# Kernel tuning notes

Measured on AMD Instinct MI355X. Metric: run time of the kernel, lower is better.

## Reference

```python
import jax, jax.numpy as jnp
import numpy as np


def setup_inputs() -> dict:
    key = jax.random.key(0)
    k1, k2, k3 = jax.random.split(key, 3)
    N, D, H, E = 8192, 1024, 1024, 16
    scale = 1.0 / np.sqrt(D)
    return {
        "x": jax.random.normal(k1, (N, D), dtype=jnp.float32),
        "router_w": jax.random.normal(k2, (D, E), dtype=jnp.float32) * scale,
        "router_b": jnp.zeros((E,), dtype=jnp.float32),
        "expert_w": jax.random.normal(k3, (E, D, H), dtype=jnp.float32) * scale,
        "expert_b": jnp.zeros((E, H), dtype=jnp.float32),
        "k": 2,
    }


def reference(x, router_w, router_b, expert_w, expert_b, k):
    # Router: softmax over experts, then top-k.
    logits = x @ router_w + router_b                      # [N, E]
    routing_weights = jax.nn.softmax(logits, axis=-1)     # [N, E]
    top_k_weights, top_k_indices = jax.lax.top_k(routing_weights, k)  # [N, k]

    # Dense all-expert compute (faithful to original): [N, E, H]
    expert_outputs = jnp.einsum('nd,edh->neh', x, expert_w) + expert_b[None, :, :]

    # Gather top-k expert outputs: [N, k, H]
    gathered = jnp.take_along_axis(expert_outputs, top_k_indices[:, :, None], axis=1)

    # Weighted sum over k (weights NOT renormalized, as in the original).
    out = jnp.sum(top_k_weights[:, :, None] * gathered, axis=1)  # [N, H]
    return out
```

## Files before the change

kernel.cpp:

```cpp
#include <hip/hip_runtime.h>
#include <hip/hip_bf16.h>


#define N_TOK 8192
#define D_DIM 1024
#define H_DIM 1024
#define E_NUM 16
#define CAP   1024
#define KPAD  40

typedef __attribute__((ext_vector_type(4))) float f32x4;
typedef __attribute__((ext_vector_type(8))) short bf16x8;

__device__ __forceinline__ unsigned short f2bf(float f) {
    unsigned int u = __float_as_uint(f);
    unsigned int r = u + 0x7fffu + ((u >> 16) & 1u);
    return (unsigned short)(r >> 16);
}
__device__ __forceinline__ unsigned int pk2bf(float lo, float hi) {
    return (unsigned int)f2bf(lo) | ((unsigned int)f2bf(hi) << 16);
}

__global__ __launch_bounds__(256) void router_lds(
    const float* __restrict__ x,
    const float* __restrict__ rw,
    const float* __restrict__ rb,
    int4* __restrict__ res,
    unsigned short* __restrict__ xb)
{
    __shared__ __align__(16) float xls[8][4][260];
    __shared__ double lg[4][2][E_NUM];

    const int tid = threadIdx.x;
    const int t0b = blockIdx.x * 8;

    {
        const int r   = tid >> 5;
        const int c32 = (tid & 31) * 32;
        const int s   = c32 >> 8;
        const int p0  = c32 & 255;
        const float* src = x + (size_t)(t0b + r) * D_DIM + c32;
        float4 v[8];
#pragma unroll
        for (int j = 0; j < 8; ++j) v[j] = *(const float4*)(src + j * 4);
#pragma unroll
        for (int j = 0; j < 8; ++j)
            *(float4*)&xls[r][s][p0 + j * 4] = v[j];
        unsigned int q[16];
#pragma unroll
        for (int j = 0; j < 8; ++j) {
            q[2 * j]     = pk2bf(v[j].x, v[j].y);
            q[2 * j + 1] = pk2bf(v[j].z, v[j].w);
        }
        unsigned short* dst = xb + (size_t)(t0b + r) * D_DIM + c32;
        *(uint4*)(dst)      = *(uint4*)&q[0];
        *(uint4*)(dst + 8)  = *(uint4*)&q[4];
        *(uint4*)(dst + 16) = *(uint4*)&q[8];
        *(uint4*)(dst + 24) = *(uint4*)&q[12];
    }
    __syncthreads();

    const int wave = tid >> 6;
    const int lane = tid & 63;
    const int ds   = lane >> 4;
    const int e    = lane & 15;
    const int lr0  = wave * 2;
    const float* rwp = rw + ds * 4096 + e;

    double acc0 = 0.0, acc1 = 0.0;
#pragma unroll 2
    for (int g = 0; g < 8; ++g) {
        float s0 = 0.0f, s1 = 0.0f;
#pragma unroll
        for (int u = 0; u < 8; ++u) {
            const int jb = g * 8 + u;
            const float4 a = *(const float4*)&xls[lr0][ds][jb * 4];
            const float4 b = *(const float4*)&xls[lr0 + 1][ds][jb * 4];
            const float w0 = rwp[jb * 64];
            const float w1 = rwp[jb * 64 + 16];
            const float w2 = rwp[jb * 64 + 32];
            const float w3 = rwp[jb * 64 + 48];
            s0 = fmaf(a.w, w3, fmaf(a.z, w2, fmaf(a.y, w1, fmaf(a.x, w0, s0))));
            s1 = fmaf(b.w, w3, fmaf(b.z, w2, fmaf(b.y, w1, fmaf(b.x, w0, s1))));
        }
        acc0 += (double)s0;
        acc1 += (double)s1;
    }

    double v0 = acc0, v1 = acc1;
    v0 += __shfl_xor(v0, 16); v0 += __shfl_xor(v0, 32);
    v1 += __shfl_xor(v1, 16); v1 += __shfl_xor(v1, 32);

    if (ds == 0) {
        const double bias = (double)rb[e];
        lg[wave][0][e] = v0 + bias;
        lg[wave][1][e] = v1 + bias;
    }
    __syncthreads();

    if (lane < 2) {
        const double* L = lg[wave][lane];
        double m = L[0];
#pragma unroll
        for (int k = 1; k < E_NUM; ++k) m = fmax(m, L[k]);

        int e1 = 0;
#pragma unroll
        for (int k = 1; k < E_NUM; ++k) if (L[k] > L[e1]) e1 = k;
        int e2 = (e1 == 0) ? 1 : 0;
        for (int k = 0; k < E_NUM; ++k)
            if (k != e1 && L[k] > L[e2]) e2 = k;

        float s = 0.0f;
#pragma unroll
        for (int k = 0; k < E_NUM; ++k) s = fmaf(expf((float)(L[k] - m)), 1.0f, s);
        const float w1 = expf((float)(L[e1] - m)) / s;
        const float w2 = expf((float)(L[e2] - m)) / s;

        const int n = t0b + wave * 2 + lane;
        res[n] = make_int4(e1, e2, __float_as_int(w1), __float_as_int(w2));
    }
}

template <bool WRITE_XB>
__global__ __launch_bounds__(256, 4) void router_kernel(
    const float* __restrict__ x,
    const float* __restrict__ rw,
    const float* __restrict__ rb,
    int4* __restrict__ res,
    unsigned short* __restrict__ xb)
{
    const int wave = threadIdx.x >> 6;
    const int lane = threadIdx.x & 63;
    const int ds   = lane >> 4;
    const int e    = lane & 15;
    const int t0   = blockIdx.x * 8 + wave * 2;

    const float* x0  = x + (size_t)t0 * D_DIM + ds * 256;
    const float* x1  = x0 + D_DIM;
    const float* rwp = rw + ds * 4096 + e;

    double acc0 = 0.0, acc1 = 0.0;
#pragma unroll 2
    for (int g = 0; g < 8; ++g) {
        float s0 = 0.0f, s1 = 0.0f;
#pragma unroll
        for (int u = 0; u < 8; ++u) {
            const int jb = g * 8 + u;
            const float4 a = *(const float4*)(x0 + jb * 4);
            const float4 b = *(const float4*)(x1 + jb * 4);
            const float w0 = rwp[jb * 64];
            const float w1 = rwp[jb * 64 + 16];
            const float w2 = rwp[jb * 64 + 32];
            const float w3 = rwp[jb * 64 + 48];
            s0 = fmaf(a.w, w3, fmaf(a.z, w2, fmaf(a.y, w1, fmaf(a.x, w0, s0))));
            s1 = fmaf(b.w, w3, fmaf(b.z, w2, fmaf(b.y, w1, fmaf(b.x, w0, s1))));
        }
        acc0 += (double)s0;
        acc1 += (double)s1;
    }

    if (WRITE_XB) {
#pragma unroll
        for (int t = 0; t < 2; ++t) {
            const float* src = x + (size_t)(t0 + t) * D_DIM + lane * 16;
            unsigned short* dst = xb + (size_t)(t0 + t) * D_DIM + lane * 16;
            const float4 v0 = *(const float4*)(src);
            const float4 v1 = *(const float4*)(src + 4);
            const float4 v2 = *(const float4*)(src + 8);
            const float4 v3 = *(const float4*)(src + 12);
            uint4 lo, hi;
            lo.x = pk2bf(v0.x, v0.y); lo.y = pk2bf(v0.z, v0.w);
            lo.z = pk2bf(v1.x, v1.y); lo.w = pk2bf(v1.z, v1.w);
            hi.x = pk2bf(v2.x, v2.y); hi.y = pk2bf(v2.z, v2.w);
            hi.z = pk2bf(v3.x, v3.y); hi.w = pk2bf(v3.z, v3.w);
            *(uint4*)dst       = lo;
            *(uint4*)(dst + 8) = hi;
        }
    }

    double v0 = acc0, v1 = acc1;
    v0 += __shfl_xor(v0, 16); v0 += __shfl_xor(v0, 32);
    v1 += __shfl_xor(v1, 16); v1 += __shfl_xor(v1, 32);

    __shared__ double lg[4][2][E_NUM];
    if (ds == 0) {
        const double bias = (double)rb[e];
        lg[wave][0][e] = v0 + bias;
        lg[wave][1][e] = v1 + bias;
    }
    __syncthreads();

    if (lane < 2) {
        const double* L = lg[wave][lane];
        double m = L[0];
#pragma unroll
        for (int k = 1; k < E_NUM; ++k) m = fmax(m, L[k]);

        int e1 = 0;
#pragma unroll
        for (int k = 1; k < E_NUM; ++k) if (L[k] > L[e1]) e1 = k;
        int e2 = (e1 == 0) ? 1 : 0;
        for (int k = 0; k < E_NUM; ++k)
            if (k != e1 && L[k] > L[e2]) e2 = k;

        float s = 0.0f;
#pragma unroll
        for (int k = 0; k < E_NUM; ++k) s = fmaf(expf((float)(L[k] - m)), 1.0f, s);
        const float w1 = expf((float)(L[e1] - m)) / s;
        const float w2 = expf((float)(L[e2] - m)) / s;

        const int n = t0 + lane;
        res[n] = make_int4(e1, e2, __float_as_int(w1), __float_as_int(w2));
    }
}

__global__ __launch_bounds__(256) void build_lists(
    const int4* __restrict__ res,
    int* __restrict__ counts0, int* __restrict__ counts1,
    int2* __restrict__ entries0, int2* __restrict__ entries1)
{
    const int e = blockIdx.x;
    __shared__ int c0, c1;
    if (threadIdx.x == 0) { c0 = 0; c1 = 0; }
    __syncthreads();

    for (int i = threadIdx.x; i < N_TOK; i += 256) {
        const int4 r = res[i];
        if (r.x == e) {
            int p = atomicAdd(&c0, 1);
            if (p < CAP) entries0[e * CAP + p] = make_int2(i, r.z);
        }
        if (r.y == e) {
            int p = atomicAdd(&c1, 1);
            if (p < CAP) entries1[e * CAP + p] = make_int2(i, r.w);
        }
    }
    __syncthreads();
    if (threadIdx.x == 0) { counts0[e] = c0; counts1[e] = c1; }
}

__global__ __launch_bounds__(256) void cvt_w_kernel(
    const float* __restrict__ ew,
    unsigned short* __restrict__ wt)
{
    const int tid = threadIdx.x;
    __shared__ unsigned short Ts[64][68];
    const int wi = blockIdx.x;
    const int e  = wi >> 8;
    const int kt = (wi >> 4) & 15;
    const int ht = wi & 15;

    {
        const int kl0 = tid >> 4;
        const int hl  = (tid & 15) * 4;
        const float* src = ew + (size_t)e * (D_DIM * H_DIM)
                         + (size_t)(kt * 64 + kl0) * H_DIM + ht * 64 + hl;
#pragma unroll
        for (int i = 0; i < 4; ++i) {
            const float4 v = *(const float4*)(src + (size_t)i * 16 * H_DIM);
            ushort4 p;
            p.x = f2bf(v.x); p.y = f2bf(v.y); p.z = f2bf(v.z); p.w = f2bf(v.w);
            *(ushort4*)&Ts[kl0 + i * 16][hl] = p;
        }
    }
    __syncthreads();
    {
        const int h2 = tid >> 2;
        const int kc = (tid & 3) * 16;
        unsigned int r[8];
#pragma unroll
        for (int i = 0; i < 8; ++i)
            r[i] = (unsigned int)Ts[kc + 2 * i][h2]
                 | ((unsigned int)Ts[kc + 2 * i + 1][h2] << 16);
        unsigned short* dst = wt + (size_t)e * (D_DIM * H_DIM)
                            + (size_t)(ht * 64 + h2) * D_DIM + kt * 64 + kc;
        *(uint4*)dst       = *(uint4*)&r[0];
        *(uint4*)(dst + 8) = *(uint4*)&r[4];
    }
}

template <bool ADD>
__global__ __launch_bounds__(256) void moe_gemm_bf16(
    const unsigned short* __restrict__ xb,
    const unsigned short* __restrict__ wt,
    const float* __restrict__ eb,
    const int* __restrict__ counts,
    const int2* __restrict__ entries,
    float* __restrict__ out)
{
    int T = 0;
    for (int k = 0; k < E_NUM; ++k) {
        int c = counts[k]; if (c > CAP) c = CAP;
        T += ((c + 127) >> 7) << 3;
    }
    if ((int)blockIdx.x >= T) return;

    const int q = T >> 3, r = T & 7;
    const int xcd = blockIdx.x & 7;
    int loc = (xcd < r ? xcd * (q + 1) : r * (q + 1) + (xcd - r) * q)
            + (blockIdx.x >> 3);

    int e = 0, count = 0;
    for (; e < E_NUM; ++e) {
        int c = counts[e]; if (c > CAP) c = CAP;
        const int nb = ((c + 127) >> 7) << 3;
        if (loc < nb) { count = c; break; }
        loc -= nb;
    }
    const int i0 = (loc >> 3) * 128;
    const int h0 = (loc & 7) * 128;

    __shared__ unsigned short Xs[2][128][KPAD];
    __shared__ unsigned short Ws[2][128][KPAD];
    __shared__ int   s_tok[128];
    __shared__ float s_w[128];

    const int tid = threadIdx.x;
    if (tid < 128) {
        const int i = i0 + tid;
        if (i < count) {
            int2 en = entries[e * CAP + i];
            s_tok[tid] = en.x;
            s_w[tid] = __int_as_float(en.y);
        } else {
            s_tok[tid] = 0;
            s_w[tid] = 0.0f;
        }
    }
    __syncthreads();

    const int wave = tid >> 6;
    const int lane = tid & 63;
    const int wr = (wave >> 1) * 64;
    const int wc = (wave & 1) * 64;
    const int l15 = lane & 15;
    const int quad = lane >> 4;

    f32x4 acc[4][4] = {};

    const int row  = tid >> 1;
    const int half = (tid & 1) * 16;
    const unsigned short* xp = xb + (size_t)s_tok[row] * D_DIM + half;
    const unsigned short* wp = wt + (size_t)(e * H_DIM + h0 + row) * D_DIM + half;

    uint4 pa0 = *(const uint4*)(xp);
    uint4 pa1 = *(const uint4*)(xp + 8);
    uint4 pw0 = *(const uint4*)(wp);
    uint4 pw1 = *(const uint4*)(wp + 8);
    *(uint4*)&Xs[0][row][half]     = pa0;
    *(uint4*)&Xs[0][row][half + 8] = pa1;
    *(uint4*)&Ws[0][row][half]     = pw0;
    *(uint4*)&Ws[0][row][half + 8] = pw1;

    int cur = 0;
    for (int d0 = 0; d0 < D_DIM; d0 += 32) {
        __syncthreads();
        const bool more = (d0 + 32 < D_DIM);

        if (more) {
            pa0 = *(const uint4*)(xp + d0 + 32);
            pa1 = *(const uint4*)(xp + d0 + 40);
            pw0 = *(const uint4*)(wp + d0 + 32);
            pw1 = *(const uint4*)(wp + d0 + 40);
        }

        bf16x8 af[4], bq[4];
#pragma unroll
        for (int i = 0; i < 4; ++i)
            af[i] = *(const bf16x8*)&Xs[cur][wr + i * 16 + l15][quad * 8];
#pragma unroll
        for (int j = 0; j < 4; ++j)
            bq[j] = *(const bf16x8*)&Ws[cur][wc + j * 16 + l15][quad * 8];
#pragma unroll
        for (int i = 0; i < 4; ++i)
#pragma unroll
            for (int j = 0; j < 4; ++j)
                acc[i][j] = __builtin_amdgcn_mfma_f32_16x16x32_bf16(
                    af[i], bq[j], acc[i][j], 0, 0, 0);

        if (more) {
            const int nxt = cur ^ 1;
            *(uint4*)&Xs[nxt][row][half]     = pa0;
            *(uint4*)&Xs[nxt][row][half + 8] = pa1;
            *(uint4*)&Ws[nxt][row][half]     = pw0;
            *(uint4*)&Ws[nxt][row][half + 8] = pw1;
        }
        cur ^= 1;
    }

    float bias_j[4];
    const float* ebp = eb + e * H_DIM + h0 + wc;
#pragma unroll
    for (int j = 0; j < 4; ++j) bias_j[j] = ebp[j * 16 + l15];

#pragma unroll
    for (int i = 0; i < 4; ++i) {
#pragma unroll
        for (int r2 = 0; r2 < 4; ++r2) {
            const int orow = wr + i * 16 + quad * 4 + r2;
            if (i0 + orow < count) {
                const int tok = s_tok[orow];
                const float w = s_w[orow];
                float* op = out + (size_t)tok * H_DIM + h0 + wc + l15;
#pragma unroll
                for (int j = 0; j < 4; ++j) {
                    float v = w * (acc[i][j][r2] + bias_j[j]);
                    if (ADD) v += op[j * 16];
                    op[j * 16] = v;
                }
            }
        }
    }
}

template <bool ADD>
__global__ __launch_bounds__(256) void moe_mfma_kernel(
    const float* __restrict__ x,
    const float* __restrict__ ew,
    const float* __restrict__ eb,
    const int* __restrict__ counts,
    const int2* __restrict__ entries,
    float* __restrict__ out)
{
    const int flat = blockIdx.x;
    const int lid  = (flat & 7) * 128 + (flat >> 3);
    const int h0 = (lid & 7) * 128;
    const int i0 = ((lid >> 3) & 7) * 128;
    const int e  = lid >> 6;

    int count = counts[e];
    if (count > CAP) count = CAP;
    if (i0 >= count) return;

    __shared__ unsigned short Xs[2][128][KPAD];
    __shared__ unsigned short Ws[2][128][KPAD];
    __shared__ int   s_tok[128];
    __shared__ float s_w[128];

    const int tid = threadIdx.x;
    if (tid < 128) {
        const int i = i0 + tid;
        if (i < count) {
            int2 en = entries[e * CAP + i];
            s_tok[tid] = en.x;
            s_w[tid] = __int_as_float(en.y);
        } else {
            s_tok[tid] = 0;
            s_w[tid] = 0.0f;
        }
    }
    __syncthreads();

    const int wave = tid >> 6;
    const int lane = tid & 63;
    const int wr = (wave >> 1) * 64;
    const int wc = (wave & 1) * 64;
    const int l15 = lane & 15;
    const int quad = lane >> 4;

    f32x4 acc[4][4] = {};

    const int a_kq = (tid & 7) * 4;
    const int a_r0 = tid >> 3;
    const int b_n  = tid & 127;
    const int b_dh = (tid >> 7) * 16;

    const float* ap[4];
#pragma unroll
    for (int it = 0; it < 4; ++it)
        ap[it] = x + (size_t)s_tok[a_r0 + it * 32] * D_DIM + a_kq;
    const float* bp = ew + (size_t)e * D_DIM * H_DIM
                    + (size_t)b_dh * H_DIM + h0 + b_n;

    float4 pa[4];
    float  pb[16];
#pragma unroll
    for (int it = 0; it < 4; ++it) pa[it] = *(const float4*)(ap[it]);
#pragma unroll
    for (int i = 0; i < 16; ++i)  pb[i] = bp[(size_t)i * H_DIM];

    {
#pragma unroll
        for (int it = 0; it < 4; ++it) {
            ushort4 p;
            p.x = f2bf(pa[it].x); p.y = f2bf(pa[it].y);
            p.z = f2bf(pa[it].z); p.w = f2bf(pa[it].w);
            *(ushort4*)&Xs[0][a_r0 + it * 32][a_kq] = p;
        }
        uint4 lo, hi;
        lo.x = pk2bf(pb[0], pb[1]);   lo.y = pk2bf(pb[2], pb[3]);
        lo.z = pk2bf(pb[4], pb[5]);   lo.w = pk2bf(pb[6], pb[7]);
        hi.x = pk2bf(pb[8], pb[9]);   hi.y = pk2bf(pb[10], pb[11]);
        hi.z = pk2bf(pb[12], pb[13]); hi.w = pk2bf(pb[14], pb[15]);
        *(uint4*)&Ws[0][b_n][b_dh]     = lo;
        *(uint4*)&Ws[0][b_n][b_dh + 8] = hi;
    }

    int cur = 0;
    for (int d0 = 0; d0 < D_DIM; d0 += 32) {
        __syncthreads();
        const bool more = (d0 + 32 < D_DIM);

        if (more) {
#pragma unroll
            for (int it = 0; it < 4; ++it)
                pa[it] = *(const float4*)(ap[it] + d0 + 32);
#pragma unroll
            for (int i = 0; i < 16; ++i)
                pb[i] = bp[(size_t)(d0 + 32 + i) * H_DIM];
        }

        bf16x8 af[4], bq[4];
#pragma unroll
        for (int i = 0; i < 4; ++i)
            af[i] = *(const bf16x8*)&Xs[cur][wr + i * 16 + l15][quad * 8];
#pragma unroll
        for (int j = 0; j < 4; ++j)
            bq[j] = *(const bf16x8*)&Ws[cur][wc + j * 16 + l15][quad * 8];
#pragma unroll
        for (int i = 0; i < 4; ++i)
#pragma unroll
            for (int j = 0; j < 4; ++j)
                acc[i][j] = __builtin_amdgcn_mfma_f32_16x16x32_bf16(
                    af[i], bq[j], acc[i][j], 0, 0, 0);

        if (more) {
            const int nxt = cur ^ 1;
#pragma unroll
            for (int it = 0; it < 4; ++it) {
                ushort4 p;
                p.x = f2bf(pa[it].x); p.y = f2bf(pa[it].y);
                p.z = f2bf(pa[it].z); p.w = f2bf(pa[it].w);
                *(ushort4*)&Xs[nxt][a_r0 + it * 32][a_kq] = p;
            }
            uint4 lo, hi;
            lo.x = pk2bf(pb[0], pb[1]);   lo.y = pk2bf(pb[2], pb[3]);
            lo.z = pk2bf(pb[4], pb[5]);   lo.w = pk2bf(pb[6], pb[7]);
            hi.x = pk2bf(pb[8], pb[9]);   hi.y = pk2bf(pb[10], pb[11]);
            hi.z = pk2bf(pb[12], pb[13]); hi.w = pk2bf(pb[14], pb[15]);
            *(uint4*)&Ws[nxt][b_n][b_dh]     = lo;
            *(uint4*)&Ws[nxt][b_n][b_dh + 8] = hi;
        }
        cur ^= 1;
    }

    float bias_j[4];
    const float* ebp = eb + e * H_DIM + h0 + wc;
#pragma unroll
    for (int j = 0; j < 4; ++j) bias_j[j] = ebp[j * 16 + l15];

#pragma unroll
    for (int i = 0; i < 4; ++i) {
#pragma unroll
        for (int r2 = 0; r2 < 4; ++r2) {
            const int orow = wr + i * 16 + quad * 4 + r2;
            if (i0 + orow < count) {
                const int tok = s_tok[orow];
                const float w = s_w[orow];
                float* op = out + (size_t)tok * H_DIM + h0 + wc + l15;
#pragma unroll
                for (int j = 0; j < 4; ++j) {
                    float v = w * (acc[i][j][r2] + bias_j[j]);
                    if (ADD) v += op[j * 16];
                    op[j * 16] = v;
                }
            }
        }
    }
}

extern "C" void kernel_launch(void* const* d_in, const int* in_sizes, int n_in,
                              void* d_out, int out_size, void* d_ws, size_t ws_size,
                              hipStream_t stream)
{
    const float* x  = (const float*)d_in[0];
    const float* rw = (const float*)d_in[1];
    const float* rb = (const float*)d_in[2];
    const float* ew = (const float*)d_in[3];
    const float* eb = (const float*)d_in[4];

    char* ws = (char*)d_ws;
    int*  counts0  = (int*)ws;
    int*  counts1  = (int*)(ws + 64);
    int2* entries0 = (int2*)(ws + 1024);
    int2* entries1 = (int2*)(ws + 1024 + E_NUM * CAP * 8);

    const size_t XB_OFF = (size_t)1 << 20;
    const size_t XB_SZ  = (size_t)N_TOK * D_DIM * 2;
    const size_t WT_OFF = XB_OFF + XB_SZ;
    const size_t WT_SZ  = (size_t)E_NUM * D_DIM * H_DIM * 2;
    const bool precache = ws_size >= WT_OFF + WT_SZ;

    int4* res = (int4*)d_out;

    if (precache) {
        unsigned short* xbp = (unsigned short*)(ws + XB_OFF);
        unsigned short* wtp = (unsigned short*)(ws + WT_OFF);
        router_lds<<<N_TOK / 8, 256, 0, stream>>>(x, rw, rb, res, xbp);
        build_lists<<<E_NUM, 256, 0, stream>>>(res, counts0, counts1,
                                               entries0, entries1);
        cvt_w_kernel<<<4096, 256, 0, stream>>>(ew, wtp);
        moe_gemm_bf16<false><<<1024, 256, 0, stream>>>(
            xbp, wtp, eb, counts0, entries0, (float*)d_out);
        moe_gemm_bf16<true><<<1024, 256, 0, stream>>>(
            xbp, wtp, eb, counts1, entries1, (float*)d_out);
    } else {
        router_kernel<false><<<N_TOK / 8, 256, 0, stream>>>(x, rw, rb, res, nullptr);
        build_lists<<<E_NUM, 256, 0, stream>>>(res, counts0, counts1,
                                               entries0, entries1);
        moe_mfma_kernel<false><<<1024, 256, 0, stream>>>(
            x, ew, eb, counts0, entries0, (float*)d_out);
        moe_mfma_kernel<true><<<1024, 256, 0, stream>>>(
            x, ew, eb, counts1, entries1, (float*)d_out);
    }
}
```

Before: 270.3 us.

## Deepen GEMM global prefetch to two stages and widen transpose store coalescing

The MoE GEMM main loop now keeps two K-slices of global loads in flight in registers. It is unrolled by two with fixed LDS buffer indices, so each global load has a full extra compute step to land before it is written to shared memory. Separately, the weight transpose kernel changes its store mapping so eight threads write contiguous 16-byte chunks along each row instead of four threads writing 32 bytes each. The cost is higher register pressure from the extra prefetch registers, which may reduce occupancy.

```diff
diff --git a/kernel.cpp b/kernel.cpp
--- a/kernel.cpp
+++ b/kernel.cpp
@@ -266,17 +266,19 @@
     }
     __syncthreads();
     {
-        const int h2 = tid >> 2;
-        const int kc = (tid & 3) * 16;
-        unsigned int r[8];
-#pragma unroll
-        for (int i = 0; i < 8; ++i)
-            r[i] = (unsigned int)Ts[kc + 2 * i][h2]
-                 | ((unsigned int)Ts[kc + 2 * i + 1][h2] << 16);
-        unsigned short* dst = wt + (size_t)e * (D_DIM * H_DIM)
-                            + (size_t)(ht * 64 + h2) * D_DIM + kt * 64 + kc;
-        *(uint4*)dst       = *(uint4*)&r[0];
-        *(uint4*)(dst + 8) = *(uint4*)&r[4];
+        const int kc = (tid & 7) * 8;
+#pragma unroll
+        for (int it = 0; it < 2; ++it) {
+            const int h2 = (tid >> 3) + it * 32;
+            unsigned int r[4];
+#pragma unroll
+            for (int i = 0; i < 4; ++i)
+                r[i] = (unsigned int)Ts[kc + 2 * i][h2]
+                     | ((unsigned int)Ts[kc + 2 * i + 1][h2] << 16);
+            unsigned short* dst = wt + (size_t)e * (D_DIM * H_DIM)
+                                + (size_t)(ht * 64 + h2) * D_DIM + kt * 64 + kc;
+            *(uint4*)dst = *(uint4*)&r[0];
+        }
     }
 }
 
@@ -344,49 +346,77 @@
     const unsigned short* xp = xb + (size_t)s_tok[row] * D_DIM + half;
     const unsigned short* wp = wt + (size_t)(e * H_DIM + h0 + row) * D_DIM + half;
 
-    uint4 pa0 = *(const uint4*)(xp);
-    uint4 pa1 = *(const uint4*)(xp + 8);
-    uint4 pw0 = *(const uint4*)(wp);
-    uint4 pw1 = *(const uint4*)(wp + 8);
-    *(uint4*)&Xs[0][row][half]     = pa0;
-    *(uint4*)&Xs[0][row][half + 8] = pa1;
-    *(uint4*)&Ws[0][row][half]     = pw0;
-    *(uint4*)&Ws[0][row][half + 8] = pw1;
-
-    int cur = 0;
-    for (int d0 = 0; d0 < D_DIM; d0 += 32) {
+    uint4 xA0 = *(const uint4*)(xp);
+    uint4 xA1 = *(const uint4*)(xp + 8);
+    uint4 wA0 = *(const uint4*)(wp);
+    uint4 wA1 = *(const uint4*)(wp + 8);
+    *(uint4*)&Xs[0][row][half]     = xA0;
+    *(uint4*)&Xs[0][row][half + 8] = xA1;
+    *(uint4*)&Ws[0][row][half]     = wA0;
+    *(uint4*)&Ws[0][row][half + 8] = wA1;
+    uint4 xB0 = *(const uint4*)(xp + 32);
+    uint4 xB1 = *(const uint4*)(xp + 40);
+    uint4 wB0 = *(const uint4*)(wp + 32);
+    uint4 wB1 = *(const uint4*)(wp + 40);
+
+    for (int d0 = 0; d0 < D_DIM; d0 += 64) {
         __syncthreads();
-        const bool more = (d0 + 32 < D_DIM);
-
-        if (more) {
-            pa0 = *(const uint4*)(xp + d0 + 32);
-            pa1 = *(const uint4*)(xp + d0 + 40);
-            pw0 = *(const uint4*)(wp + d0 + 32);
-            pw1 = *(const uint4*)(wp + d0 + 40);
-        }
-
-        bf16x8 af[4], bq[4];
-#pragma unroll
-        for (int i = 0; i < 4; ++i)
-            af[i] = *(const bf16x8*)&Xs[cur][wr + i * 16 + l15][quad * 8];
-#pragma unroll
-        for (int j = 0; j < 4; ++j)
-            bq[j] = *(const bf16x8*)&Ws[cur][wc + j * 16 + l15][quad * 8];
-#pragma unroll
-        for (int i = 0; i < 4; ++i)
+        const bool mA = (d0 + 64 < D_DIM);
+        if (mA) {
+            xA0 = *(const uint4*)(xp + d0 + 64);
+            xA1 = *(const uint4*)(xp + d0 + 72);
+            wA0 = *(const uint4*)(wp + d0 + 64);
+            wA1 = *(const uint4*)(wp + d0 + 72);
+        }
+        {
+            bf16x8 af[4], bq[4];
+#pragma unroll
+            for (int i = 0; i < 4; ++i)
+                af[i] = *(const bf16x8*)&Xs[0][wr + i * 16 + l15][quad * 8];
 #pragma unroll
             for (int j = 0; j < 4; ++j)
-                acc[i][j] = __builtin_amdgcn_mfma_f32_16x16x32_bf16(
-                    af[i], bq[j], acc[i][j], 0, 0, 0);
-
-        if (more) {
-            const int nxt = cur ^ 1;
-            *(uint4*)&Xs[nxt][row][half]     = pa0;
-            *(uint4*)&Xs[nxt][row][half + 8] = pa1;
-            *(uint4*)&Ws[nxt][row][half]     = pw0;
-            *(uint4*)&Ws[nxt][row][half + 8] = pw1;
-        }
-        cur ^= 1;
+                bq[j] = *(const bf16x8*)&Ws[0][wc + j * 16 + l15][quad * 8];
+#pragma unroll
+            for (int i = 0; i < 4; ++i)
+#pragma unroll
+                for (int j = 0; j < 4; ++j)
+                    acc[i][j] = __builtin_amdgcn_mfma_f32_16x16x32_bf16(
+                        af[i], bq[j], acc[i][j], 0, 0, 0);
+        }
+        *(uint4*)&Xs[1][row][half]     = xB0;
+        *(uint4*)&Xs[1][row][half + 8] = xB1;
+        *(uint4*)&Ws[1][row][half]     = wB0;
+        *(uint4*)&Ws[1][row][half + 8] = wB1;
+
+        __syncthreads();
+        const bool mB = (d0 + 96 < D_DIM);
+        if (mB) {
+            xB0 = *(const uint4*)(xp + d0 + 96);
+            xB1 = *(const uint4*)(xp + d0 + 104);
+            wB0 = *(const uint4*)(wp + d0 + 96);
+            wB1 = *(const uint4*)(wp + d0 + 104);
+        }
+        {
+            bf16x8 af[4], bq[4];
+#pragma unroll
+            for (int i = 0; i < 4; ++i)
+                af[i] = *(const bf16x8*)&Xs[1][wr + i * 16 + l15][quad * 8];
+#pragma unroll
+            for (int j = 0; j < 4; ++j)
+                bq[j] = *(const bf16x8*)&Ws[1][wc + j * 16 + l15][quad * 8];
+#pragma unroll
+            for (int i = 0; i < 4; ++i)
+#pragma unroll
+                for (int j = 0; j < 4; ++j)
+                    acc[i][j] = __builtin_amdgcn_mfma_f32_16x16x32_bf16(
+                        af[i], bq[j], acc[i][j], 0, 0, 0);
+        }
+        if (mA) {
+            *(uint4*)&Xs[0][row][half]     = xA0;
+            *(uint4*)&Xs[0][row][half + 8] = xA1;
+            *(uint4*)&Ws[0][row][half]     = wA0;
+            *(uint4*)&Ws[0][row][half + 8] = wA1;
+        }
     }
 
     float bias_j[4];
```

Result: slower. 299.6 us (+10.8%).
